# Optimization experiments

Hardware: AMD Instinct MI355X
Metric: run time of the kernel (lower is better)

Reference implementation:

```python
import jax, jax.numpy as jnp
import numpy as np

N = 100000   # nodes
E = 300000   # edges
D = 256      # emb_dim
L = 5        # num_layers
SELF_LOOP_BOND_TYPE = 4
BN_EPS = 1e-5


def setup_inputs() -> dict:
    key = jax.random.key(0)
    ks = jax.random.split(key, 12)
    s = 0.05
    x = jax.random.randint(ks[0], (N, 2), 0, 3)
    edge_index = jax.random.randint(ks[1], (2, E), 0, N)
    edge_attr = jax.random.randint(ks[2], (E, 2), 0, 3)
    x_emb1 = jax.random.normal(ks[3], (120, D), dtype=jnp.float32) * s
    x_emb2 = jax.random.normal(ks[4], (3, D), dtype=jnp.float32) * s
    edge_emb1 = jax.random.normal(ks[5], (L, 6, D), dtype=jnp.float32) * s
    edge_emb2 = jax.random.normal(ks[6], (L, 3, D), dtype=jnp.float32) * s
    W1 = jax.random.normal(ks[7], (L, D, 2 * D), dtype=jnp.float32) * (1.0 / np.sqrt(D))
    b1 = jnp.zeros((L, 2 * D), dtype=jnp.float32)
    W2 = jax.random.normal(ks[8], (L, 2 * D, D), dtype=jnp.float32) * (1.0 / np.sqrt(2 * D))
    b2 = jnp.zeros((L, D), dtype=jnp.float32)
    bn_gamma = jnp.ones((L - 1, D), dtype=jnp.float32)
    bn_beta = jnp.zeros((L - 1, D), dtype=jnp.float32)
    return dict(x=x, edge_index=edge_index, edge_attr=edge_attr,
                x_emb1=x_emb1, x_emb2=x_emb2,
                edge_emb1=edge_emb1, edge_emb2=edge_emb2,
                W1=W1, b1=b1, W2=W2, b2=b2,
                bn_gamma=bn_gamma, bn_beta=bn_beta)


def reference(x, edge_index, edge_attr, x_emb1, x_emb2, edge_emb1, edge_emb2,
              W1, b1, W2, b2, bn_gamma, bn_beta):
    n = x.shape[0]
    loop = jnp.arange(n)
    # add_self_loops: append (i, i) for every node
    src = jnp.concatenate([edge_index[0], loop])  # [E+N]
    dst = jnp.concatenate([edge_index[1], loop])  # [E+N]
    # self-loop edge_attr = (bond_type=4, direction=0)
    self_attr = jnp.concatenate([
        jnp.full((n, 1), SELF_LOOP_BOND_TYPE, dtype=edge_attr.dtype),
        jnp.zeros((n, 1), dtype=edge_attr.dtype)], axis=1)
    ea = jnp.concatenate([edge_attr, self_attr], axis=0)  # [E+N, 2]

    out = x_emb1[x[:, 0]] + x_emb2[x[:, 1]]  # [N, D]
    for l in range(L):
        e_emb = edge_emb1[l][ea[:, 0]] + edge_emb2[l][ea[:, 1]]  # [E+N, D]
        msg = out[src] + e_emb                                   # gather + message
        agg = jax.ops.segment_sum(msg, dst, num_segments=n)      # scatter-add
        h = jax.nn.relu(agg @ W1[l] + b1[l]) @ W2[l] + b2[l]     # GIN MLP
        if l < L - 1:
            mean = h.mean(axis=0)
            var = h.var(axis=0)  # biased var, matches torch BN training
            h = (h - mean) * jax.lax.rsqrt(var + BN_EPS) * bn_gamma[l] + bn_beta[l]
            h = jax.nn.relu(h)
        out = h
    return out
```

## Files before the change

### kernel.cpp

```cpp
#include <hip/hip_runtime.h>

typedef unsigned short u16;
typedef unsigned int u32;

#define DD 256

typedef short  s16x8 __attribute__((ext_vector_type(8)));
typedef short  s16x4 __attribute__((ext_vector_type(4)));
typedef float  f32x4 __attribute__((ext_vector_type(4)));

__device__ __forceinline__ float b2f(u16 u){
  union { u32 i; float f; } c; c.i = ((u32)u) << 16; return c.f;
}
__device__ __forceinline__ u16 f2b(float f){
  union { float f; u32 i; } c; c.f = f;
  u32 b = c.i + 0x7FFFu + ((c.i >> 16) & 1u);
  return (u16)(b >> 16);
}

__global__ void NodeEncoder_72971494359603_kernel(){}

__global__ void probe_dtype(const u32* w, u32* flag){
  if (threadIdx.x == 0 && blockIdx.x == 0){
    int cnt = 0;
    for (int i = 0; i < 256; i++){
      u32 low = w[i] & 0xFFFFu;
      u32 e = (low >> 7) & 0xFFu;
      if (e >= 0x60u && e <= 0x7Eu) cnt++;
    }
    *flag = (cnt >= 192) ? 1u : 0u;
  }
}

__global__ void cvt_in(const void* src, u16* dst, int n, const u32* flag){
  int i = blockIdx.x * 256 + threadIdx.x;
  if (i < n){
    if (*flag){
      dst[i] = ((const u16*)src)[i];
    } else {
      dst[i] = f2b(((const float*)src)[i]);
    }
  }
}

__global__ void store_out(const u16* h, void* dout, int n, const u32* flag){
  int i = blockIdx.x * 256 + threadIdx.x;
  if (i < n){
    if (*flag){
      ((u16*)dout)[i] = h[i];
    } else {
      ((float*)dout)[i] = b2f(h[i]);
    }
  }
}

__global__ void zero_int(int* p, int n){
  int i = blockIdx.x * 256 + threadIdx.x;
  if (i < n) p[i] = 0;
}

__global__ void build_table(const u16* ee1, const u16* ee2, float* TBL){
  int b = blockIdx.x;
  int l = b / 18, c = b % 18, a = c / 3, bb = c % 3;
  int j = threadIdx.x;
  TBL[b * DD + j] = b2f(ee1[(l * 6 + a) * DD + j]) + b2f(ee2[(l * 3 + bb) * DD + j]);
}

__global__ void hist_kernel(const int* dst, int* counts, int E){
  int e = blockIdx.x * 256 + threadIdx.x;
  if (e < E) atomicAdd(&counts[dst[e]], 1);
}

__global__ void scan_sums(const int* counts, int* bsum, int N){
  __shared__ int red[256];
  int tid = threadIdx.x;
  int base = blockIdx.x * 1024;
  int s = 0;
  for (int i = tid; i < 1024; i += 256){
    int g = base + i;
    if (g < N) s += counts[g];
  }
  red[tid] = s;
  __syncthreads();
  for (int off = 128; off > 0; off >>= 1){
    if (tid < off) red[tid] += red[tid + off];
    __syncthreads();
  }
  if (tid == 0) bsum[blockIdx.x] = red[0];
}

__global__ void scan_top(int* bsum, int nb){
  if (threadIdx.x == 0 && blockIdx.x == 0){
    int acc = 0;
    for (int i = 0; i < nb; i++){ int t = bsum[i]; bsum[i] = acc; acc += t; }
  }
}

__global__ void scan_block(const int* counts, const int* bsum,
                           int* offsets, int* cursor, int N){
  __shared__ int tsum[256];
  int b = blockIdx.x;
  int tid = threadIdx.x;
  int base = b * 1024;
  int v0, v1, v2, v3;
  int g = base + tid * 4;
  v0 = (g + 0 < N) ? counts[g + 0] : 0;
  v1 = (g + 1 < N) ? counts[g + 1] : 0;
  v2 = (g + 2 < N) ? counts[g + 2] : 0;
  v3 = (g + 3 < N) ? counts[g + 3] : 0;
  tsum[tid] = v0 + v1 + v2 + v3;
  __syncthreads();
  for (int off = 1; off < 256; off <<= 1){
    int t = (tid >= off) ? tsum[tid - off] : 0;
    __syncthreads();
    tsum[tid] += t;
    __syncthreads();
  }
  int excl = (tid == 0 ? 0 : tsum[tid - 1]) + bsum[b];
  if (g + 0 < N){ offsets[g + 0] = excl; cursor[g + 0] = excl; } excl += v0;
  if (g + 1 < N){ offsets[g + 1] = excl; cursor[g + 1] = excl; } excl += v1;
  if (g + 2 < N){ offsets[g + 2] = excl; cursor[g + 2] = excl; } excl += v2;
  if (g + 3 < N){ offsets[g + 3] = excl; cursor[g + 3] = excl; }
}

__global__ void fill_csr(const int* ei, const int* ea, int* cursor,
                         int* payload, int E){
  int e = blockIdx.x * 256 + threadIdx.x;
  if (e < E){
    int d = ei[E + e];
    int pos = atomicAdd(&cursor[d], 1);
    int a = ea[2 * e], bb = ea[2 * e + 1];
    payload[pos] = ei[e] | ((a * 3 + bb) << 17);
  }
}

__global__ void node_embed(const int* x, const u16* xe1, const u16* xe2,
                           u16* out, int N){
  int idx = blockIdx.x * 256 + threadIdx.x;
  if (idx < N * DD){
    int n = idx >> 8, j = idx & 255;
    int x0 = x[2 * n], x1 = x[2 * n + 1];
    out[idx] = f2b(b2f(xe1[x0 * DD + j]) + b2f(xe2[x1 * DD + j]));
  }
}

__global__ void pack_B(const u16* __restrict__ W0, u16* __restrict__ Wp0, int K, int Nc){
  const u16* W = W0 + (size_t)blockIdx.y * K * Nc;
  u16* Wp = Wp0 + (size_t)blockIdx.y * K * Nc;
  int idx = blockIdx.x * 256 + threadIdx.x;
  int lane = idx & 63;
  int t = idx >> 6;
  int nk = K >> 5;
  int ksub = t % nk, cblk = t / nk;
  if (cblk >= (Nc >> 4)) return;
  int col = cblk * 16 + (lane & 15);
  int krow = ksub * 32 + (lane >> 4) * 8;
  u16* dst = Wp + (size_t)idx * 8;
#pragma unroll
  for (int e = 0; e < 8; e++)
    dst[e] = W[(size_t)(krow + e) * Nc + col];
}

__global__ __launch_bounds__(512, 4)
void layer_fused(const u16* __restrict__ feat, const float* __restrict__ TBL,
                 const int* __restrict__ offsets, const int* __restrict__ counts,
                 const int* __restrict__ payload,
                 const u16* __restrict__ Wp1, const u16* __restrict__ bias1,
                 const u16* __restrict__ Wp2, const u16* __restrict__ bias2,
                 u16* __restrict__ H, float* __restrict__ partial, int npart, int M,
                 const float* __restrict__ sums, const u16* __restrict__ gamma,
                 const u16* __restrict__ beta, float invN, int apply_bn){
  __shared__ __align__(16) u16 As[64 * 256];
  __shared__ __align__(16) u16 Ms[2][64 * 128];
  float* T = (float*)Ms;
  int tid = threadIdx.x, lane = tid & 63, wave = tid >> 6;
  int wr = wave >> 2, wc = wave & 3;
  int row0 = blockIdx.x * 64;
  int lr = lane & 15, hi = lane >> 4;

  for (int i = tid; i < 18 * DD; i += 512) T[i] = TBL[i];
  __syncthreads();

  {
    int c4 = lane * 4;
    float sc[4], sh[4];
    if (apply_bn){
#pragma unroll
      for (int e = 0; e < 4; e++){
        int j = c4 + e;
        float mean = sums[j] * invN;
        float var = sums[DD + j] * invN - mean * mean;
        if (var < 0.f) var = 0.f;
        float scl = rsqrtf(var + 1e-5f) * b2f(gamma[j]);
        sc[e] = scl; sh[e] = b2f(beta[j]) - mean * scl;
      }
    } else {
#pragma unroll
      for (int e = 0; e < 4; e++){ sc[e] = 1.f; sh[e] = 0.f; }
    }
    for (int u = 0; u < 8; u++){
      int r = wave * 8 + u;
      int n = row0 + r; if (n > M - 1) n = M - 1;
      s16x4 sv = *(const s16x4*)(feat + (size_t)n * DD + c4);
      f32x4 tb = *(const f32x4*)(T + 12 * DD + c4);
      float v0 = b2f((u16)sv[0]) * sc[0] + sh[0];
      float v1 = b2f((u16)sv[1]) * sc[1] + sh[1];
      float v2 = b2f((u16)sv[2]) * sc[2] + sh[2];
      float v3 = b2f((u16)sv[3]) * sc[3] + sh[3];
      if (apply_bn){
        v0 = fmaxf(v0, 0.f); v1 = fmaxf(v1, 0.f);
        v2 = fmaxf(v2, 0.f); v3 = fmaxf(v3, 0.f);
      }
      float a0 = v0 + tb[0], a1 = v1 + tb[1], a2 = v2 + tb[2], a3 = v3 + tb[3];
      int e0 = offsets[n], cnt = counts[n];
      for (int e = e0; e < e0 + cnt; e++){
        int pl = payload[e];
        int src = pl & 0x1FFFF;
        int idx = pl >> 17;
        s16x4 rv = *(const s16x4*)(feat + (size_t)src * DD + c4);
        f32x4 tv = *(const f32x4*)(T + idx * DD + c4);
        float w0 = b2f((u16)rv[0]) * sc[0] + sh[0];
        float w1 = b2f((u16)rv[1]) * sc[1] + sh[1];
        float w2 = b2f((u16)rv[2]) * sc[2] + sh[2];
        float w3 = b2f((u16)rv[3]) * sc[3] + sh[3];
        if (apply_bn){
          w0 = fmaxf(w0, 0.f); w1 = fmaxf(w1, 0.f);
          w2 = fmaxf(w2, 0.f); w3 = fmaxf(w3, 0.f);
        }
        a0 += w0 + tv[0];
        a1 += w1 + tv[1];
        a2 += w2 + tv[2];
        a3 += w3 + tv[3];
      }
      s16x4 o;
      o[0] = (short)f2b(a0); o[1] = (short)f2b(a1);
      o[2] = (short)f2b(a2); o[3] = (short)f2b(a3);
      int byteo = r * 512 + ((((lane >> 1) ^ (r & 7)) & 31) << 4) + ((lane & 1) << 3);
      *(s16x4*)((char*)As + byteo) = o;
    }
  }
  __syncthreads();

  f32x4 zero = {0.f, 0.f, 0.f, 0.f};
  f32x4 acc2[2][4];
#pragma unroll
  for (int m = 0; m < 2; m++)
#pragma unroll
    for (int n = 0; n < 4; n++) acc2[m][n] = zero;
  f32x4 acc1[2][2];

  auto G1 = [&](int cc){
#pragma unroll
    for (int m = 0; m < 2; m++)
#pragma unroll
      for (int n = 0; n < 2; n++) acc1[m][n] = zero;
#pragma unroll
    for (int ks = 0; ks < 8; ks++){
      s16x8 af[2];
#pragma unroll
      for (int m = 0; m < 2; m++){
        int arow = wr * 32 + m * 16 + lr;
        af[m] = *(const s16x8*)((const char*)As + arow * 512 +
                                ((ks * 64 + hi * 16) ^ ((arow & 7) << 4)));
      }
#pragma unroll
      for (int n = 0; n < 2; n++){
        int cb = cc * 8 + wc * 2 + n;
        s16x8 bf = *(const s16x8*)(Wp1 + (((size_t)cb * 8 + ks) * 64 + lane) * 8);
        acc1[0][n] = __builtin_amdgcn_mfma_f32_16x16x32_bf16(af[0], bf, acc1[0][n], 0, 0, 0);
        acc1[1][n] = __builtin_amdgcn_mfma_f32_16x16x32_bf16(af[1], bf, acc1[1][n], 0, 0, 0);
      }
    }
  };
  auto WMS = [&](int cc, int buf){
    char* ms = (char*)Ms[buf];
#pragma unroll
    for (int n = 0; n < 2; n++){
      float bv = b2f(bias1[cc * 128 + wc * 32 + n * 16 + lr]);
      int c2 = (wc * 32 + n * 16 + lr) * 2;
#pragma unroll
      for (int m = 0; m < 2; m++)
#pragma unroll
        for (int r = 0; r < 4; r++){
          int mrow = wr * 32 + m * 16 + hi * 4 + r;
          float v = fmaxf(acc1[m][n][r] + bv, 0.f);
          *(u16*)(ms + mrow * 256 + (c2 ^ ((mrow & 7) << 4))) = f2b(v);
        }
    }
  };

  G1(0);
  WMS(0, 0);
  __syncthreads();

#pragma unroll
  for (int c = 0; c < 4; c++){
    const char* ms = (const char*)Ms[c & 1];
#pragma unroll
    for (int ks = 0; ks < 4; ks++){
      s16x8 mf[2];
#pragma unroll
      for (int m = 0; m < 2; m++){
        int mrow = wr * 32 + m * 16 + lr;
        mf[m] = *(const s16x8*)(ms + mrow * 256 +
                                ((ks * 64 + hi * 16) ^ ((mrow & 7) << 4)));
      }
#pragma unroll
      for (int n = 0; n < 4; n++){
        int cb2 = wc * 4 + n;
        s16x8 wf = *(const s16x8*)(Wp2 + (((size_t)cb2 * 16 + c * 4 + ks) * 64 + lane) * 8);
        acc2[0][n] = __builtin_amdgcn_mfma_f32_16x16x32_bf16(mf[0], wf, acc2[0][n], 0, 0, 0);
        acc2[1][n] = __builtin_amdgcn_mfma_f32_16x16x32_bf16(mf[1], wf, acc2[1][n], 0, 0, 0);
      }
    }
    if (c < 3){
      G1(c + 1);
      WMS(c + 1, (c + 1) & 1);
      __syncthreads();
    }
  }

#pragma unroll
  for (int n = 0; n < 4; n++){
    float bv = b2f(bias2[wc * 64 + n * 16 + lr]);
    int c2 = (wc * 64 + n * 16 + lr) * 2;
#pragma unroll
    for (int m = 0; m < 2; m++)
#pragma unroll
      for (int r = 0; r < 4; r++){
        int mrow = wr * 32 + m * 16 + hi * 4 + r;
        *(u16*)((char*)As + mrow * 512 + (c2 ^ ((mrow & 7) << 4))) = f2b(acc2[m][n][r] + bv);
      }
  }
  __syncthreads();

  float s[8], q[8];
#pragma unroll
  for (int e = 0; e < 8; e++){ s[e] = 0.f; q[e] = 0.f; }
  int sl = tid & 31;
#pragma unroll
  for (int p = 0; p < 4; p++){
    int r = p * 16 + (tid >> 5);
    s16x8 v = *(const s16x8*)((const char*)As + r * 512 + ((sl << 4) ^ ((r & 7) << 4)));
    int gr = row0 + r;
    if (gr < M){
      *(s16x8*)(H + (size_t)gr * DD + sl * 8) = v;
      if (partial){
#pragma unroll
        for (int e = 0; e < 8; e++){
          float f = b2f((u16)v[e]);
          s[e] += f; q[e] += f * f;
        }
      }
    }
  }
  if (partial){
#pragma unroll
    for (int e = 0; e < 8; e++){
      s[e] += __shfl_xor(s[e], 32);
      q[e] += __shfl_xor(q[e], 32);
    }
    float* redS = (float*)Ms;
    float* redQ = redS + 8 * 256;
    if (lane < 32){
#pragma unroll
      for (int e = 0; e < 8; e++){
        redS[wave * 256 + sl * 8 + e] = s[e];
        redQ[wave * 256 + sl * 8 + e] = q[e];
      }
    }
    __syncthreads();
    if (tid < 256){
      float a = 0.f, b = 0.f;
#pragma unroll
      for (int w = 0; w < 8; w++){ a += redS[w * 256 + tid]; b += redQ[w * 256 + tid]; }
      partial[(size_t)blockIdx.x * DD + tid] = a;
      partial[(size_t)(npart + blockIdx.x) * DD + tid] = b;
    }
  }
}

__global__ void bn_reduce(const float* __restrict__ partial, float* __restrict__ sums,
                          int npart){
  int b = blockIdx.x, which = b >> 3, jg = b & 7;
  int t = threadIdx.x;
  int j = jg * 32 + (t >> 3);
  int li = t & 7;
  float s = 0.f;
  for (int i = li; i < npart; i += 8)
    s += partial[(size_t)(which * npart + i) * DD + j];
  s += __shfl_xor(s, 1); s += __shfl_xor(s, 2); s += __shfl_xor(s, 4);
  if (li == 0) sums[which * DD + j] = s;
}

extern "C" void kernel_launch(void* const* d_in, const int* in_sizes, int n_in,
                              void* d_out, int out_size, void* d_ws, size_t ws_size,
                              hipStream_t stream){
  (void)n_in; (void)out_size; (void)ws_size;
  const int* x    = (const int*)d_in[0];
  const int* ei   = (const int*)d_in[1];
  const int* ea   = (const int*)d_in[2];
  const void* xe1 = d_in[3];
  const void* xe2 = d_in[4];
  const void* ee1 = d_in[5];
  const void* ee2 = d_in[6];
  const void* W1  = d_in[7];
  const void* b1  = d_in[8];
  const void* W2  = d_in[9];
  const void* b2  = d_in[10];
  const void* gam = d_in[11];
  const void* bet = d_in[12];

  int N = in_sizes[0] / 2;
  int E = in_sizes[1] / 2;
  int NB = (N + 1023) / 1024;
  const int L = 5;
  int nblk = (N + 63) / 64;
  int npart = nblk;

  char* base = (char*)d_ws;
  size_t off = 0;
  u32* flag    = (u32*)(base + off);   off += 256;
  float* TBL   = (float*)(base + off); off += ((size_t)L * 18 * DD * 4 + 255) & ~(size_t)255;
  int* counts  = (int*)(base + off);   off += ((size_t)N * 4 + 255) & ~(size_t)255;
  int* offsets = (int*)(base + off);   off += ((size_t)N * 4 + 255) & ~(size_t)255;
  int* cursor  = (int*)(base + off);   off += ((size_t)N * 4 + 255) & ~(size_t)255;
  int* bsum    = (int*)(base + off);   off += ((size_t)NB * 4 + 255) & ~(size_t)255;
  int* payload = (int*)(base + off);   off += ((size_t)E * 4 + 255) & ~(size_t)255;
  float* part  = (float*)(base + off); off += ((size_t)2 * npart * DD * 4 + 255) & ~(size_t)255;
  float* sums  = (float*)(base + off); off += ((size_t)2 * DD * 4 + 255) & ~(size_t)255;
  u16* wx1  = (u16*)(base + off); off += ((size_t)120 * DD * 2 + 255) & ~(size_t)255;
  u16* wx2  = (u16*)(base + off); off += ((size_t)3 * DD * 2 + 255) & ~(size_t)255;
  u16* wee1 = (u16*)(base + off); off += ((size_t)L * 6 * DD * 2 + 255) & ~(size_t)255;
  u16* wee2 = (u16*)(base + off); off += ((size_t)L * 3 * DD * 2 + 255) & ~(size_t)255;
  u16* wW1  = (u16*)(base + off); off += ((size_t)L * DD * 2 * DD * 2 + 255) & ~(size_t)255;
  u16* wb1  = (u16*)(base + off); off += ((size_t)L * 2 * DD * 2 + 255) & ~(size_t)255;
  u16* wW2  = (u16*)(base + off); off += ((size_t)L * 2 * DD * DD * 2 + 255) & ~(size_t)255;
  u16* wb2  = (u16*)(base + off); off += ((size_t)L * DD * 2 + 255) & ~(size_t)255;
  u16* wgam = (u16*)(base + off); off += ((size_t)(L - 1) * DD * 2 + 255) & ~(size_t)255;
  u16* wbet = (u16*)(base + off); off += ((size_t)(L - 1) * DD * 2 + 255) & ~(size_t)255;
  u16* Wp1  = (u16*)(base + off); off += ((size_t)L * DD * 2 * DD * 2 + 255) & ~(size_t)255;
  u16* Wp2  = (u16*)(base + off); off += ((size_t)L * 2 * DD * DD * 2 + 255) & ~(size_t)255;
  u16* featA = (u16*)(base + off); off += ((size_t)N * DD * 2 + 255) & ~(size_t)255;
  u16* featB = (u16*)(base + off); off += ((size_t)N * DD * 2 + 255) & ~(size_t)255;

  probe_dtype<<<1, 64, 0, stream>>>((const u32*)xe1, flag);
  cvt_in<<<(120 * DD + 255) / 256, 256, 0, stream>>>(xe1, wx1, 120 * DD, flag);
  cvt_in<<<(3 * DD + 255) / 256, 256, 0, stream>>>(xe2, wx2, 3 * DD, flag);
  cvt_in<<<(L * 6 * DD + 255) / 256, 256, 0, stream>>>(ee1, wee1, L * 6 * DD, flag);
  cvt_in<<<(L * 3 * DD + 255) / 256, 256, 0, stream>>>(ee2, wee2, L * 3 * DD, flag);
  cvt_in<<<(L * DD * 2 * DD + 255) / 256, 256, 0, stream>>>(W1, wW1, L * DD * 2 * DD, flag);
  cvt_in<<<(L * 2 * DD + 255) / 256, 256, 0, stream>>>(b1, wb1, L * 2 * DD, flag);
  cvt_in<<<(L * 2 * DD * DD + 255) / 256, 256, 0, stream>>>(W2, wW2, L * 2 * DD * DD, flag);
  cvt_in<<<(L * DD + 255) / 256, 256, 0, stream>>>(b2, wb2, L * DD, flag);
  cvt_in<<<((L - 1) * DD + 255) / 256, 256, 0, stream>>>(gam, wgam, (L - 1) * DD, flag);
  cvt_in<<<((L - 1) * DD + 255) / 256, 256, 0, stream>>>(bet, wbet, (L - 1) * DD, flag);

  build_table<<<90, 256, 0, stream>>>(wee1, wee2, TBL);
  pack_B<<<dim3(64, L), 256, 0, stream>>>(wW1, Wp1, DD, 2 * DD);
  pack_B<<<dim3(64, L), 256, 0, stream>>>(wW2, Wp2, 2 * DD, DD);
  zero_int<<<(N + 255) / 256, 256, 0, stream>>>(counts, N);
  hist_kernel<<<(E + 255) / 256, 256, 0, stream>>>(ei + E, counts, E);
  scan_sums<<<NB, 256, 0, stream>>>(counts, bsum, N);
  scan_top<<<1, 64, 0, stream>>>(bsum, NB);
  scan_block<<<NB, 256, 0, stream>>>(counts, bsum, offsets, cursor, N);
  fill_csr<<<(E + 255) / 256, 256, 0, stream>>>(ei, ea, cursor, payload, E);

  node_embed<<<(N * DD + 255) / 256, 256, 0, stream>>>(x, wx1, wx2, featA, N);

  float invN = 1.0f / (float)N;
  u16* fin = featA;
  u16* fout = featB;

  for (int l = 0; l < L; l++){
    layer_fused<<<nblk, 512, 0, stream>>>(
        fin, TBL + (size_t)l * 18 * DD, offsets, counts, payload,
        Wp1 + (size_t)l * DD * 2 * DD, wb1 + (size_t)l * 2 * DD,
        Wp2 + (size_t)l * 2 * DD * DD, wb2 + (size_t)l * DD,
        fout, (l < L - 1) ? part : (float*)nullptr, npart, N,
        sums, wgam + (size_t)(l > 0 ? l - 1 : 0) * DD,
        wbet + (size_t)(l > 0 ? l - 1 : 0) * DD, invN, l > 0 ? 1 : 0);

    if (l < L - 1){
      bn_reduce<<<16, 256, 0, stream>>>(part, sums, npart);
    }
    u16* t = fin; fin = fout; fout = t;
  }

  store_out<<<(N * DD + 255) / 256, 256, 0, stream>>>(fin, d_out, N * DD, flag);
}
```

Measured before the change: 1.646 ms.

## Shrink fused layer block to 32 rows, prefetch gathers, keep A fragments in registers

The fused GIN layer kernel moves from 512 threads over 64 rows to 256 threads over 32 rows, with one wave per column group. Shared memory drops to a single 16KB buffer that is reused for the aggregated A tile, the double-buffered MLP hidden tile, the output staging and the BN reduction. The edge table is no longer staged in LDS and is read from global/L1 instead. The A-operand fragments are loaded into registers once, and the neighbor gather loop software-prefetches the next edge's row. The goal is to cut LDS footprint for higher occupancy and to hide gather latency, at the cost of more registers, twice as many blocks and partial sums, and more weight reloads per row.

```diff
diff --git a/kernel.cpp b/kernel.cpp
--- a/kernel.cpp
+++ b/kernel.cpp
@@ -161,7 +161,7 @@
     dst[e] = W[(size_t)(krow + e) * Nc + col];
 }
 
-__global__ __launch_bounds__(512, 4)
+__global__ __launch_bounds__(256, 4)
 void layer_fused(const u16* __restrict__ feat, const float* __restrict__ TBL,
                  const int* __restrict__ offsets, const int* __restrict__ counts,
                  const int* __restrict__ payload,
@@ -170,16 +170,11 @@
                  u16* __restrict__ H, float* __restrict__ partial, int npart, int M,
                  const float* __restrict__ sums, const u16* __restrict__ gamma,
                  const u16* __restrict__ beta, float invN, int apply_bn){
-  __shared__ __align__(16) u16 As[64 * 256];
-  __shared__ __align__(16) u16 Ms[2][64 * 128];
-  float* T = (float*)Ms;
+  __shared__ __align__(16) char LB[16384];
   int tid = threadIdx.x, lane = tid & 63, wave = tid >> 6;
-  int wr = wave >> 2, wc = wave & 3;
-  int row0 = blockIdx.x * 64;
+  int wc = wave;
+  int row0 = blockIdx.x * 32;
   int lr = lane & 15, hi = lane >> 4;
-
-  for (int i = tid; i < 18 * DD; i += 512) T[i] = TBL[i];
-  __syncthreads();
 
   {
     int c4 = lane * 4;
@@ -202,7 +197,7 @@
       int r = wave * 8 + u;
       int n = row0 + r; if (n > M - 1) n = M - 1;
       s16x4 sv = *(const s16x4*)(feat + (size_t)n * DD + c4);
-      f32x4 tb = *(const f32x4*)(T + 12 * DD + c4);
+      f32x4 tb = *(const f32x4*)(TBL + 12 * DD + c4);
       float v0 = b2f((u16)sv[0]) * sc[0] + sh[0];
       float v1 = b2f((u16)sv[1]) * sc[1] + sh[1];
       float v2 = b2f((u16)sv[2]) * sc[2] + sh[2];
@@ -212,32 +207,50 @@
         v2 = fmaxf(v2, 0.f); v3 = fmaxf(v3, 0.f);
       }
       float a0 = v0 + tb[0], a1 = v1 + tb[1], a2 = v2 + tb[2], a3 = v3 + tb[3];
-      int e0 = offsets[n], cnt = counts[n];
-      for (int e = e0; e < e0 + cnt; e++){
-        int pl = payload[e];
-        int src = pl & 0x1FFFF;
-        int idx = pl >> 17;
-        s16x4 rv = *(const s16x4*)(feat + (size_t)src * DD + c4);
-        f32x4 tv = *(const f32x4*)(T + idx * DD + c4);
-        float w0 = b2f((u16)rv[0]) * sc[0] + sh[0];
-        float w1 = b2f((u16)rv[1]) * sc[1] + sh[1];
-        float w2 = b2f((u16)rv[2]) * sc[2] + sh[2];
-        float w3 = b2f((u16)rv[3]) * sc[3] + sh[3];
-        if (apply_bn){
-          w0 = fmaxf(w0, 0.f); w1 = fmaxf(w1, 0.f);
-          w2 = fmaxf(w2, 0.f); w3 = fmaxf(w3, 0.f);
+      int e0 = offsets[n], cnt = counts[n], eend = e0 + cnt;
+      if (cnt > 0){
+        int pl = payload[e0];
+        s16x4 rv = *(const s16x4*)(feat + (size_t)(pl & 0x1FFFF) * DD + c4);
+        f32x4 tv = *(const f32x4*)(TBL + (pl >> 17) * DD + c4);
+        for (int e = e0; e < eend; e++){
+          int pln = 0; s16x4 rvn; f32x4 tvn;
+          if (e + 1 < eend){
+            pln = payload[e + 1];
+            rvn = *(const s16x4*)(feat + (size_t)(pln & 0x1FFFF) * DD + c4);
+            tvn = *(const f32x4*)(TBL + (pln >> 17) * DD + c4);
+          }
+          float w0 = b2f((u16)rv[0]) * sc[0] + sh[0];
+          float w1 = b2f((u16)rv[1]) * sc[1] + sh[1];
+          float w2 = b2f((u16)rv[2]) * sc[2] + sh[2];
+          float w3 = b2f((u16)rv[3]) * sc[3] + sh[3];
+          if (apply_bn){
+            w0 = fmaxf(w0, 0.f); w1 = fmaxf(w1, 0.f);
+            w2 = fmaxf(w2, 0.f); w3 = fmaxf(w3, 0.f);
+          }
+          a0 += w0 + tv[0];
+          a1 += w1 + tv[1];
+          a2 += w2 + tv[2];
+          a3 += w3 + tv[3];
+          rv = rvn; tv = tvn;
         }
-        a0 += w0 + tv[0];
-        a1 += w1 + tv[1];
-        a2 += w2 + tv[2];
-        a3 += w3 + tv[3];
       }
       s16x4 o;
       o[0] = (short)f2b(a0); o[1] = (short)f2b(a1);
       o[2] = (short)f2b(a2); o[3] = (short)f2b(a3);
       int byteo = r * 512 + ((((lane >> 1) ^ (r & 7)) & 31) << 4) + ((lane & 1) << 3);
-      *(s16x4*)((char*)As + byteo) = o;
-    }
+      *(s16x4*)(LB + byteo) = o;
+    }
+  }
+  __syncthreads();
+
+  s16x8 af[2][8];
+#pragma unroll
+  for (int m = 0; m < 2; m++){
+    int arow = m * 16 + lr;
+#pragma unroll
+    for (int ks = 0; ks < 8; ks++)
+      af[m][ks] = *(const s16x8*)(LB + arow * 512 +
+                                  ((ks * 64 + hi * 16) ^ ((arow & 7) << 4)));
   }
   __syncthreads();
 
@@ -256,24 +269,17 @@
       for (int n = 0; n < 2; n++) acc1[m][n] = zero;
 #pragma unroll
     for (int ks = 0; ks < 8; ks++){
-      s16x8 af[2];
-#pragma unroll
-      for (int m = 0; m < 2; m++){
-        int arow = wr * 32 + m * 16 + lr;
-        af[m] = *(const s16x8*)((const char*)As + arow * 512 +
-                                ((ks * 64 + hi * 16) ^ ((arow & 7) << 4)));
-      }
 #pragma unroll
       for (int n = 0; n < 2; n++){
         int cb = cc * 8 + wc * 2 + n;
         s16x8 bf = *(const s16x8*)(Wp1 + (((size_t)cb * 8 + ks) * 64 + lane) * 8);
-        acc1[0][n] = __builtin_amdgcn_mfma_f32_16x16x32_bf16(af[0], bf, acc1[0][n], 0, 0, 0);
-        acc1[1][n] = __builtin_amdgcn_mfma_f32_16x16x32_bf16(af[1], bf, acc1[1][n], 0, 0, 0);
+        acc1[0][n] = __builtin_amdgcn_mfma_f32_16x16x32_bf16(af[0][ks], bf, acc1[0][n], 0, 0, 0);
+        acc1[1][n] = __builtin_amdgcn_mfma_f32_16x16x32_bf16(af[1][ks], bf, acc1[1][n], 0, 0, 0);
       }
     }
   };
   auto WMS = [&](int cc, int buf){
-    char* ms = (char*)Ms[buf];
+    char* ms = LB + buf * 8192;
 #pragma unroll
     for (int n = 0; n < 2; n++){
       float bv = b2f(bias1[cc * 128 + wc * 32 + n * 16 + lr]);
@@ -282,7 +288,7 @@
       for (int m = 0; m < 2; m++)
 #pragma unroll
         for (int r = 0; r < 4; r++){
-          int mrow = wr * 32 + m * 16 + hi * 4 + r;
+          int mrow = m * 16 + hi * 4 + r;
           float v = fmaxf(acc1[m][n][r] + bv, 0.f);
           *(u16*)(ms + mrow * 256 + (c2 ^ ((mrow & 7) << 4))) = f2b(v);
         }
@@ -295,13 +301,13 @@
 
 #pragma unroll
   for (int c = 0; c < 4; c++){
-    const char* ms = (const char*)Ms[c & 1];
+    const char* ms = LB + (c & 1) * 8192;
 #pragma unroll
     for (int ks = 0; ks < 4; ks++){
       s16x8 mf[2];
 #pragma unroll
       for (int m = 0; m < 2; m++){
-        int mrow = wr * 32 + m * 16 + lr;
+        int mrow = m * 16 + lr;
         mf[m] = *(const s16x8*)(ms + mrow * 256 +
                                 ((ks * 64 + hi * 16) ^ ((mrow & 7) << 4)));
       }
@@ -316,8 +322,8 @@
     if (c < 3){
       G1(c + 1);
       WMS(c + 1, (c + 1) & 1);
-      __syncthreads();
-    }
+    }
+    __syncthreads();
   }
 
 #pragma unroll
@@ -328,8 +334,8 @@
     for (int m = 0; m < 2; m++)
 #pragma unroll
       for (int r = 0; r < 4; r++){
-        int mrow = wr * 32 + m * 16 + hi * 4 + r;
-        *(u16*)((char*)As + mrow * 512 + (c2 ^ ((mrow & 7) << 4))) = f2b(acc2[m][n][r] + bv);
+        int mrow = m * 16 + hi * 4 + r;
+        *(u16*)(LB + mrow * 512 + (c2 ^ ((mrow & 7) << 4))) = f2b(acc2[m][n][r] + bv);
       }
   }
   __syncthreads();
@@ -340,8 +346,8 @@
   int sl = tid & 31;
 #pragma unroll
   for (int p = 0; p < 4; p++){
-    int r = p * 16 + (tid >> 5);
-    s16x8 v = *(const s16x8*)((const char*)As + r * 512 + ((sl << 4) ^ ((r & 7) << 4)));
+    int r = p * 8 + (tid >> 5);
+    s16x8 v = *(const s16x8*)(LB + r * 512 + ((sl << 4) ^ ((r & 7) << 4)));
     int gr = row0 + r;
     if (gr < M){
       *(s16x8*)(H + (size_t)gr * DD + sl * 8) = v;
@@ -360,8 +366,9 @@
       s[e] += __shfl_xor(s[e], 32);
       q[e] += __shfl_xor(q[e], 32);
     }
-    float* redS = (float*)Ms;
-    float* redQ = redS + 8 * 256;
+    __syncthreads();
+    float* redS = (float*)LB;
+    float* redQ = redS + 4 * 256;
     if (lane < 32){
 #pragma unroll
       for (int e = 0; e < 8; e++){
@@ -370,13 +377,11 @@
       }
     }
     __syncthreads();
-    if (tid < 256){
-      float a = 0.f, b = 0.f;
-#pragma unroll
-      for (int w = 0; w < 8; w++){ a += redS[w * 256 + tid]; b += redQ[w * 256 + tid]; }
-      partial[(size_t)blockIdx.x * DD + tid] = a;
-      partial[(size_t)(npart + blockIdx.x) * DD + tid] = b;
-    }
+    float a = 0.f, b = 0.f;
+#pragma unroll
+    for (int w = 0; w < 4; w++){ a += redS[w * 256 + tid]; b += redQ[w * 256 + tid]; }
+    partial[(size_t)blockIdx.x * DD + tid] = a;
+    partial[(size_t)(npart + blockIdx.x) * DD + tid] = b;
   }
 }
 
@@ -415,7 +420,7 @@
   int E = in_sizes[1] / 2;
   int NB = (N + 1023) / 1024;
   const int L = 5;
-  int nblk = (N + 63) / 64;
+  int nblk = (N + 31) / 32;
   int npart = nblk;
 
   char* base = (char*)d_ws;
@@ -473,7 +478,7 @@
   u16* fout = featB;
 
   for (int l = 0; l < L; l++){
-    layer_fused<<<nblk, 512, 0, stream>>>(
+    layer_fused<<<nblk, 256, 0, stream>>>(
         fin, TBL + (size_t)l * 18 * DD, offsets, counts, payload,
         Wp1 + (size_t)l * DD * 2 * DD, wb1 + (size_t)l * 2 * DD,
         Wp2 + (size_t)l * 2 * DD * DD, wb2 + (size_t)l * DD,
```

After: 2.185 ms. +32.8%, slower.
